# Kernel tuning notes

Measured on AMD Instinct MI355X. Metric: run time of the kernel, lower is better.

## Reference

```python
import jax, jax.numpy as jnp
import numpy as np

NEG_SLOPE = 0.2


def gat_conv(x, src, dst, W, att_src, att_dst, bias, heads, out_ch, concat, N):
    # Linear transform: [N, heads, out_ch]
    h = (x @ W).reshape(N, heads, out_ch)
    # Per-node attention logits [N, heads]
    a_s = jnp.einsum('nhc,hc->nh', h, att_src)
    a_d = jnp.einsum('nhc,hc->nh', h, att_dst)
    # Per-edge logits: edge j->i uses src j, dst i
    e = jax.nn.leaky_relu(a_s[src] + a_d[dst], NEG_SLOPE)  # [E, heads]
    # Segment softmax over destination neighborhoods
    m = jax.ops.segment_max(e, dst, num_segments=N)  # [N, heads]
    ex = jnp.exp(e - m[dst])
    denom = jax.ops.segment_sum(ex, dst, num_segments=N)
    alpha = ex / denom[dst]  # [E, heads]
    # Weighted message scatter-add
    out = jax.ops.segment_sum(h[src] * alpha[:, :, None], dst, num_segments=N)  # [N, heads, out_ch]
    out = out.reshape(N, heads * out_ch) if concat else out.mean(axis=1)
    return out + bias


def setup_inputs() -> dict:
    key = jax.random.key(0)
    ks = jax.random.split(key, 12)
    N, E, F_IN, HID, HEADS, NCLS = 100000, 1600000, 256, 16, 8, 32
    x = jax.random.normal(ks[0], (N, F_IN), dtype=jnp.float32)
    edge_index = jax.random.randint(ks[1], (2, E), 0, N, dtype=jnp.int32)
    edge_weight = jax.random.uniform(ks[2], (E,), dtype=jnp.float32)
    s1 = 1.0 / np.sqrt(F_IN)
    W1 = jax.random.normal(ks[3], (F_IN, HEADS * HID), dtype=jnp.float32) * s1
    att_src1 = jax.random.normal(ks[4], (HEADS, HID), dtype=jnp.float32) * 0.1
    att_dst1 = jax.random.normal(ks[5], (HEADS, HID), dtype=jnp.float32) * 0.1
    b1 = jnp.zeros((HEADS * HID,), dtype=jnp.float32)
    s2 = 1.0 / np.sqrt(HEADS * HID)
    W2 = jax.random.normal(ks[6], (HEADS * HID, NCLS), dtype=jnp.float32) * s2
    att_src2 = jax.random.normal(ks[7], (1, NCLS), dtype=jnp.float32) * 0.1
    att_dst2 = jax.random.normal(ks[8], (1, NCLS), dtype=jnp.float32) * 0.1
    b2 = jnp.zeros((NCLS,), dtype=jnp.float32)
    return {"x": x, "edge_index": edge_index, "edge_weight": edge_weight,
            "W1": W1, "att_src1": att_src1, "att_dst1": att_dst1, "b1": b1,
            "W2": W2, "att_src2": att_src2, "att_dst2": att_dst2, "b2": b2}


def reference(x, edge_index, edge_weight, W1, att_src1, att_dst1, b1, W2, att_src2, att_dst2, b2):
    N = x.shape[0]
    # PyG GATConv add_self_loops=True: append self-loops once (used by both layers)
    loop = jnp.arange(N, dtype=edge_index.dtype)
    src = jnp.concatenate([edge_index[0], loop])
    dst = jnp.concatenate([edge_index[1], loop])
    # eval mode: dropout is identity; edge_weight unused by GATConv
    h = gat_conv(x, src, dst, W1, att_src1, att_dst1, b1, heads=8, out_ch=16, concat=True, N=N)
    h = jax.nn.elu(h)
    out = gat_conv(h, src, dst, W2, att_src2, att_dst2, b2, heads=1, out_ch=32, concat=False, N=N)
    return jax.nn.log_softmax(out, axis=-1)
```

## Files before the change

kernel.cpp:

```cpp
#include <hip/hip_runtime.h>
#include <hip/hip_fp16.h>
#include <math.h>

#define NEG_SLOPE 0.2f
#define NBLK 256

typedef _Float16 half8 __attribute__((ext_vector_type(8)));
typedef _Float16 half4 __attribute__((ext_vector_type(4)));
typedef float f32x4 __attribute__((ext_vector_type(4)));

__device__ __forceinline__ float lrelu(float x){ return x > 0.f ? x : NEG_SLOPE*x; }

__global__ void k_prepw(const float* __restrict__ W, _Float16* __restrict__ Wt){
  int t = blockIdx.x*blockDim.x + threadIdx.x;
  int c = t >> 8, k = t & 255;
  Wt[t] = (_Float16)W[k*128 + c];
}

__global__ __launch_bounds__(256) void k_gemm1(const float* __restrict__ x,
                                               const _Float16* __restrict__ Wt,
                                               _Float16* __restrict__ h1h, int N){
  __shared__ _Float16 aL[2][128*40];
  __shared__ _Float16 bL[2][128*40];
  int tid = threadIdx.x;
  int w = tid >> 6, lane = tid & 63;
  int fq = lane >> 4, fr = lane & 15;
  int row0 = blockIdx.x * 128;
  f32x4 acc[2][8];
  #pragma unroll
  for (int m=0;m<2;m++)
    #pragma unroll
    for (int n=0;n<8;n++) acc[m][n] = (f32x4){0.f,0.f,0.f,0.f};

  int rA = tid>>3, kcA = (tid&7)*4;
  float4 va[4]; half8 vb[2];

  #pragma unroll
  for (int it=0; it<4; it++){
    int gr = row0 + it*32 + rA;
    va[it] = make_float4(0.f,0.f,0.f,0.f);
    if (gr < N) va[it] = *(const float4*)&x[(size_t)gr*256 + kcA];
  }
  #pragma unroll
  for (int it=0; it<2; it++){
    int chunk = it*256 + tid;
    vb[it] = *(const half8*)&Wt[(size_t)(chunk>>2)*256 + (chunk&3)*8];
  }
  #pragma unroll
  for (int it=0; it<4; it++){
    half4 hv; hv[0]=(_Float16)va[it].x; hv[1]=(_Float16)va[it].y;
    hv[2]=(_Float16)va[it].z; hv[3]=(_Float16)va[it].w;
    *(half4*)&aL[0][(it*32+rA)*40 + kcA] = hv;
  }
  #pragma unroll
  for (int it=0; it<2; it++){
    int chunk = it*256 + tid;
    *(half8*)&bL[0][(chunk>>2)*40 + (chunk&3)*8] = vb[it];
  }
  __syncthreads();

  int cur = 0;
  for (int ki=0; ki<8; ki++){
    int kk = ki*32;
    if (ki < 7){
      #pragma unroll
      for (int it=0; it<4; it++){
        int gr = row0 + it*32 + rA;
        va[it] = make_float4(0.f,0.f,0.f,0.f);
        if (gr < N) va[it] = *(const float4*)&x[(size_t)gr*256 + kk + 32 + kcA];
      }
      #pragma unroll
      for (int it=0; it<2; it++){
        int chunk = it*256 + tid;
        vb[it] = *(const half8*)&Wt[(size_t)(chunk>>2)*256 + kk + 32 + (chunk&3)*8];
      }
    }
    int kb = fq*8;
    half8 afrag[2], bfrag[8];
    #pragma unroll
    for (int m=0;m<2;m++) afrag[m] = *(half8*)&aL[cur][(w*32 + m*16 + fr)*40 + kb];
    #pragma unroll
    for (int n=0;n<8;n++) bfrag[n] = *(half8*)&bL[cur][(n*16 + fr)*40 + kb];
    #pragma unroll
    for (int m=0;m<2;m++)
      #pragma unroll
      for (int n=0;n<8;n++)
        acc[m][n] = __builtin_amdgcn_mfma_f32_16x16x32_f16(afrag[m], bfrag[n], acc[m][n], 0, 0, 0);
    if (ki < 7){
      #pragma unroll
      for (int it=0; it<4; it++){
        half4 hv; hv[0]=(_Float16)va[it].x; hv[1]=(_Float16)va[it].y;
        hv[2]=(_Float16)va[it].z; hv[3]=(_Float16)va[it].w;
        *(half4*)&aL[cur^1][(it*32+rA)*40 + kcA] = hv;
      }
      #pragma unroll
      for (int it=0; it<2; it++){
        int chunk = it*256 + tid;
        *(half8*)&bL[cur^1][(chunk>>2)*40 + (chunk&3)*8] = vb[it];
      }
      __syncthreads();
      cur ^= 1;
    }
  }
  #pragma unroll
  for (int m=0;m<2;m++){
    #pragma unroll
    for (int j=0;j<4;j++){
      int gr = row0 + w*32 + m*16 + fq*4 + j;
      if (gr < N){
        #pragma unroll
        for (int n=0;n<8;n++)
          h1h[(size_t)gr*128 + n*16 + fr] = (_Float16)acc[m][n][j];
      }
    }
  }
}

__global__ void k_att1(const __half* __restrict__ h1h, const float* __restrict__ as_w,
                       const float* __restrict__ ad_w,
                       float* __restrict__ a_s, float* __restrict__ a_d, int N){
  int t = blockIdx.x*blockDim.x + threadIdx.x;
  if (t >= N*8) return;
  int n = t >> 3, h = t & 7;
  const __half* hp = &h1h[(size_t)n*128 + h*16];
  const float* wsp = &as_w[h*16];
  const float* wdp = &ad_w[h*16];
  float s=0.f, d=0.f;
  #pragma unroll
  for (int j=0;j<8;j++){
    __half2 hv = *(const __half2*)&hp[j*2];
    float2 f = __half22float2(hv);
    s = fmaf(f.x, wsp[j*2],   s); d = fmaf(f.x, wdp[j*2],   d);
    s = fmaf(f.y, wsp[j*2+1], s); d = fmaf(f.y, wdp[j*2+1], d);
  }
  a_s[t] = s; a_d[t] = d;
}

__global__ __launch_bounds__(256) void k_bh(const int* __restrict__ dst, int* __restrict__ bh,
                                            int E, int EE, int NB){
  __shared__ int h[1024];
  int tid = threadIdx.x, blk = blockIdx.x;
  for (int i=tid;i<1024;i+=256) h[i]=0;
  __syncthreads();
  int chunk = (EE + NBLK - 1)/NBLK;
  int e0 = blk*chunk, e1 = min(e0+chunk, EE);
  for (int e=e0+tid; e<e1; e+=256){
    int d = (e<E)? dst[e] : (e-E);
    atomicAdd(&h[d>>7], 1);
  }
  __syncthreads();
  for (int i=tid;i<NB;i+=256) bh[i*NBLK + blk] = h[i];
}

__global__ __launch_bounds__(256) void k_scanA(int* __restrict__ bh, int* __restrict__ btot){
  __shared__ int t[256];
  int b = blockIdx.x, tid = threadIdx.x;
  int v = bh[b*NBLK + tid];
  t[tid] = v;
  __syncthreads();
  for (int off=1; off<256; off<<=1){
    int p = (tid>=off)? t[tid-off] : 0;
    __syncthreads();
    t[tid] += p;
    __syncthreads();
  }
  bh[b*NBLK + tid] = t[tid] - v;
  if (tid==255) btot[b] = t[255];
}

__global__ __launch_bounds__(256) void k_bscan(const int* __restrict__ btot, int* __restrict__ bbase,
                                               int* __restrict__ start_, int NB, int N, int EE){
  __shared__ int t[256];
  int tid = threadIdx.x;
  int i0 = tid*4;
  int a0 = (i0+0<NB)? btot[i0+0] : 0;
  int a1 = (i0+1<NB)? btot[i0+1] : 0;
  int a2 = (i0+2<NB)? btot[i0+2] : 0;
  int a3 = (i0+3<NB)? btot[i0+3] : 0;
  int s = a0+a1+a2+a3;
  t[tid] = s;
  __syncthreads();
  for (int off=1; off<256; off<<=1){
    int p = (tid>=off)? t[tid-off] : 0;
    __syncthreads();
    t[tid] += p;
    __syncthreads();
  }
  int excl = t[tid] - s;
  int e0=excl, e1=e0+a0, e2=e1+a1, e3=e2+a2;
  if (i0+0<NB) bbase[i0+0]=e0;
  if (i0+1<NB) bbase[i0+1]=e1;
  if (i0+2<NB) bbase[i0+2]=e2;
  if (i0+3<NB) bbase[i0+3]=e3;
  if (tid==0){ bbase[NB] = EE; start_[N] = EE; }
}

__global__ __launch_bounds__(256) void k_bfill(const int* __restrict__ src, const int* __restrict__ dst,
                       const int* __restrict__ bh, const int* __restrict__ bbase,
                       uint2* __restrict__ pairs, int E, int EE, int NB){
  __shared__ int cur[1024];
  int tid = threadIdx.x, blk = blockIdx.x;
  for (int i=tid;i<NB;i+=256) cur[i] = bbase[i] + bh[i*NBLK + blk];
  __syncthreads();
  int chunk = (EE + NBLK - 1)/NBLK;
  int e0 = blk*chunk, e1 = min(e0+chunk, EE);
  for (int e=e0+tid; e<e1; e+=256){
    int s,d;
    if (e<E){ s=src[e]; d=dst[e]; } else { s=e-E; d=s; }
    int p = atomicAdd(&cur[d>>7], 1);
    pairs[p] = make_uint2((unsigned)s,(unsigned)d);
  }
}

__global__ __launch_bounds__(256) void k_pb(const int* __restrict__ bbase, const uint2* __restrict__ pairs,
                    int* __restrict__ start_, int* __restrict__ csr_src, int N){
  __shared__ int hist[128];
  __shared__ int excl[128];
  int b = blockIdx.x;
  int tid = threadIdx.x;
  int base = bbase[b], cnt = bbase[b+1] - base;
  if (tid<128) hist[tid]=0;
  __syncthreads();
  for (int i=tid;i<cnt;i+=256){
    uint2 p = pairs[base+i];
    atomicAdd(&hist[p.y & 127], 1);
  }
  __syncthreads();
  if (tid < 128) excl[tid] = hist[tid];
  __syncthreads();
  for (int off=1; off<128; off<<=1){
    int p=0;
    if (tid<128 && tid>=off) p = excl[tid-off];
    __syncthreads();
    if (tid<128) excl[tid] += p;
    __syncthreads();
  }
  if (tid < 128){
    int e = excl[tid] - hist[tid];
    int node = (b<<7) + tid;
    if (node < N) start_[node] = base + e;
    hist[tid] = e;
  }
  __syncthreads();
  for (int i=tid;i<cnt;i+=256){
    uint2 p = pairs[base+i];
    int pos = atomicAdd(&hist[p.y & 127], 1);
    csr_src[base + pos] = (int)p.x;
  }
}

__global__ __launch_bounds__(256) void k_agg1(const int* __restrict__ start, const int* __restrict__ csr_src,
                      const float* __restrict__ a_s, const float* __restrict__ a_d,
                      const __half* __restrict__ h1h, float* __restrict__ acc1, int N){
  int wid = (blockIdx.x*blockDim.x + threadIdx.x) >> 6;
  int lane = threadIdx.x & 63;
  if (wid >= N) return;
  int d = wid;
  int half = lane >> 5;
  int l32  = lane & 31;
  int head = l32 >> 2;
  float ad = a_d[(size_t)d*8 + head];
  int beg = start[d], end = start[d+1];
  float ax=0.f, ay=0.f, az=0.f, aw=0.f, den=0.f;
  int j = beg + half;
  for (; j + 6 < end; j += 8){
    int s0 = csr_src[j];
    int s1 = csr_src[j+2];
    int s2 = csr_src[j+4];
    int s3 = csr_src[j+6];
    float e0 = __expf(lrelu(a_s[(size_t)s0*8 + head] + ad));
    float e1 = __expf(lrelu(a_s[(size_t)s1*8 + head] + ad));
    float e2 = __expf(lrelu(a_s[(size_t)s2*8 + head] + ad));
    float e3 = __expf(lrelu(a_s[(size_t)s3*8 + head] + ad));
    float2 r0 = *(const float2*)&h1h[(size_t)s0*128 + l32*4];
    float2 r1 = *(const float2*)&h1h[(size_t)s1*128 + l32*4];
    float2 r2 = *(const float2*)&h1h[(size_t)s2*128 + l32*4];
    float2 r3 = *(const float2*)&h1h[(size_t)s3*128 + l32*4];
    float2 f0a = __half22float2(*(__half2*)&r0.x), f0b = __half22float2(*(__half2*)&r0.y);
    float2 f1a = __half22float2(*(__half2*)&r1.x), f1b = __half22float2(*(__half2*)&r1.y);
    float2 f2a = __half22float2(*(__half2*)&r2.x), f2b = __half22float2(*(__half2*)&r2.y);
    float2 f3a = __half22float2(*(__half2*)&r3.x), f3b = __half22float2(*(__half2*)&r3.y);
    ax = fmaf(e0, f0a.x, ax); ay = fmaf(e0, f0a.y, ay); az = fmaf(e0, f0b.x, az); aw = fmaf(e0, f0b.y, aw);
    ax = fmaf(e1, f1a.x, ax); ay = fmaf(e1, f1a.y, ay); az = fmaf(e1, f1b.x, az); aw = fmaf(e1, f1b.y, aw);
    ax = fmaf(e2, f2a.x, ax); ay = fmaf(e2, f2a.y, ay); az = fmaf(e2, f2b.x, az); aw = fmaf(e2, f2b.y, aw);
    ax = fmaf(e3, f3a.x, ax); ay = fmaf(e3, f3a.y, ay); az = fmaf(e3, f3b.x, az); aw = fmaf(e3, f3b.y, aw);
    den += (e0 + e1) + (e2 + e3);
  }
  for (; j < end; j += 2){
    int s0 = csr_src[j];
    float e0 = __expf(lrelu(a_s[(size_t)s0*8 + head] + ad));
    float2 r0 = *(const float2*)&h1h[(size_t)s0*128 + l32*4];
    float2 f0a = __half22float2(*(__half2*)&r0.x), f0b = __half22float2(*(__half2*)&r0.y);
    ax = fmaf(e0, f0a.x, ax); ay = fmaf(e0, f0a.y, ay); az = fmaf(e0, f0b.x, az); aw = fmaf(e0, f0b.y, aw);
    den += e0;
  }
  ax += __shfl_xor(ax, 32);
  ay += __shfl_xor(ay, 32);
  az += __shfl_xor(az, 32);
  aw += __shfl_xor(aw, 32);
  den += __shfl_xor(den, 32);
  float inv = (den > 0.f) ? 1.f/den : 0.f;
  if (half == 0){
    float4 o = make_float4(ax*inv, ay*inv, az*inv, aw*inv);
    *(float4*)&acc1[(size_t)d*128 + l32*4] = o;
  }
}

__global__ __launch_bounds__(256) void k_layer2(const float* __restrict__ acc1, const float* __restrict__ b1,
                        const float* __restrict__ W2, const float* __restrict__ as2w,
                        const float* __restrict__ ad2w,
                        __half* __restrict__ h2ph, float* __restrict__ a_s2,
                        float* __restrict__ a_d2, int N){
  __shared__ float w2s[128][32];
  __shared__ float hs[8][128];
  int tid = threadIdx.x;
  #pragma unroll
  for (int it=0; it<16; it++){
    int idx = it*256 + tid;
    ((float*)w2s)[idx] = W2[idx];
  }
  int sub = tid>>5, ln = tid&31;
  int n = blockIdx.x*8 + sub;
  if (n < N){
    #pragma unroll
    for (int j=0;j<4;j++){
      int k = j*32 + ln;
      float v = acc1[(size_t)n*128+k] + b1[k];
      hs[sub][k] = v > 0.f ? v : (__expf(v) - 1.f);
    }
  }
  __syncthreads();
  if (n >= N) return;
  float o = 0.f;
  #pragma unroll
  for (int k=0;k<128;k++) o = fmaf(hs[sub][k], w2s[k][ln], o);
  h2ph[(size_t)n*32+ln] = __float2half_rn(o);
  float ps = o*as2w[ln], pd = o*ad2w[ln];
  #pragma unroll
  for (int m=16;m;m>>=1){ ps += __shfl_xor(ps,m); pd += __shfl_xor(pd,m); }
  if (ln==0){ a_s2[n]=ps; a_d2[n]=pd; }
}

__global__ __launch_bounds__(256) void k_agg2(const int* __restrict__ start, const int* __restrict__ csr_src,
                      const float* __restrict__ a_s2, const float* __restrict__ a_d2,
                      const __half* __restrict__ h2ph, const float* __restrict__ b2,
                      float* __restrict__ out, int N){
  int g = (blockIdx.x*blockDim.x + threadIdx.x) >> 5;
  int ln = threadIdx.x & 31;
  if (g >= N) return;
  int d = g;
  int grp = ln >> 4;
  int l16 = ln & 15;
  float ad = a_d2[d];
  int beg = start[d], end = start[d+1];
  float accx=0.f, accy=0.f, den=0.f;
  int j = beg + grp;
  for (; j + 6 < end; j += 8){
    int s0 = csr_src[j];
    int s1 = csr_src[j+2];
    int s2 = csr_src[j+4];
    int s3 = csr_src[j+6];
    float e0 = __expf(lrelu(a_s2[s0] + ad));
    float e1 = __expf(lrelu(a_s2[s1] + ad));
    float e2 = __expf(lrelu(a_s2[s2] + ad));
    float e3 = __expf(lrelu(a_s2[s3] + ad));
    float2 v0 = __half22float2(*(const __half2*)&h2ph[(size_t)s0*32 + l16*2]);
    float2 v1 = __half22float2(*(const __half2*)&h2ph[(size_t)s1*32 + l16*2]);
    float2 v2 = __half22float2(*(const __half2*)&h2ph[(size_t)s2*32 + l16*2]);
    float2 v3 = __half22float2(*(const __half2*)&h2ph[(size_t)s3*32 + l16*2]);
    accx = fmaf(e0, v0.x, accx); accy = fmaf(e0, v0.y, accy);
    accx = fmaf(e1, v1.x, accx); accy = fmaf(e1, v1.y, accy);
    accx = fmaf(e2, v2.x, accx); accy = fmaf(e2, v2.y, accy);
    accx = fmaf(e3, v3.x, accx); accy = fmaf(e3, v3.y, accy);
    den += (e0 + e1) + (e2 + e3);
  }
  for (; j < end; j += 2){
    int s0 = csr_src[j];
    float e0 = __expf(lrelu(a_s2[s0] + ad));
    float2 v0 = __half22float2(*(const __half2*)&h2ph[(size_t)s0*32 + l16*2]);
    accx = fmaf(e0, v0.x, accx); accy = fmaf(e0, v0.y, accy);
    den += e0;
  }
  accx += __shfl_xor(accx, 16);
  accy += __shfl_xor(accy, 16);
  den  += __shfl_xor(den, 16);
  float2 bb = *(const float2*)&b2[l16*2];
  float vx = accx/den + bb.x;
  float vy = accy/den + bb.y;
  float mx = fmaxf(vx, vy);
  #pragma unroll
  for (int m=8;m;m>>=1) mx = fmaxf(mx, __shfl_xor(mx, m));
  float sm = __expf(vx-mx) + __expf(vy-mx);
  #pragma unroll
  for (int m=8;m;m>>=1) sm += __shfl_xor(sm, m);
  float lg = mx + __logf(sm);
  if (grp == 0){
    float2 o = make_float2(vx - lg, vy - lg);
    *(float2*)&out[(size_t)d*32 + l16*2] = o;
  }
}

extern "C" void kernel_launch(void* const* d_in, const int* in_sizes, int n_in,
                              void* d_out, int out_size, void* d_ws, size_t ws_size,
                              hipStream_t stream){
  const float* x   = (const float*)d_in[0];
  const int*   ei  = (const int*)d_in[1];
  const float* W1  = (const float*)d_in[3];
  const float* as1 = (const float*)d_in[4];
  const float* ad1 = (const float*)d_in[5];
  const float* b1  = (const float*)d_in[6];
  const float* W2  = (const float*)d_in[7];
  const float* as2 = (const float*)d_in[8];
  const float* ad2 = (const float*)d_in[9];
  const float* b2  = (const float*)d_in[10];

  int N  = in_sizes[0] / 256;
  int E  = in_sizes[2];
  int EE = E + N;
  const int* src = ei;
  const int* dst = ei + E;

  int NB = (N + 127) >> 7;

  int* iw = (int*)d_ws;
  int* bh      = iw;                 iw += 1024*NBLK;
  int* btot    = iw;                 iw += 1024;
  int* bbase   = iw;                 iw += 1028;
  int* start_  = iw;                 iw += ((N+1+3)/4)*4;
  int* csr_src = iw;                 iw += ((EE+3)/4)*4;

  float* w = (float*)iw;
  float* a_s1   = w; w += (size_t)N*8;
  float* a_d1   = w; w += (size_t)N*8;
  float* acc1   = w; w += (size_t)N*128;
  float* a_s2   = w; w += (size_t)N;
  float* a_d2   = w; w += (size_t)N;
  _Float16* h1h  = (_Float16*)w; w += (size_t)N*64;
  _Float16* h2ph = (_Float16*)w; w += (size_t)N*16;
  _Float16* Wt   = (_Float16*)w; w += 32768/2;
  float* out    = (float*)d_out;

  uint2* pairs = (uint2*)acc1;

  hipLaunchKernelGGL(k_prepw, dim3(128), dim3(256), 0, stream, W1, Wt);
  hipLaunchKernelGGL(k_gemm1, dim3((N+127)/128), dim3(256), 0, stream, x, Wt, h1h, N);
  hipLaunchKernelGGL(k_att1, dim3((N*8+255)/256), dim3(256), 0, stream, (const __half*)h1h, as1, ad1, a_s1, a_d1, N);
  hipLaunchKernelGGL(k_bh,    dim3(NBLK), dim3(256), 0, stream, dst, bh, E, EE, NB);
  hipLaunchKernelGGL(k_scanA, dim3(NB),   dim3(256), 0, stream, bh, btot);
  hipLaunchKernelGGL(k_bscan, dim3(1),    dim3(256), 0, stream, btot, bbase, start_, NB, N, EE);
  hipLaunchKernelGGL(k_bfill, dim3(NBLK), dim3(256), 0, stream, src, dst, bh, bbase, pairs, E, EE, NB);
  hipLaunchKernelGGL(k_pb,    dim3(NB),   dim3(256), 0, stream, bbase, pairs, start_, csr_src, N);
  hipLaunchKernelGGL(k_agg1, dim3((N+3)/4), dim3(256), 0, stream, start_, csr_src, a_s1, a_d1, (const __half*)h1h, acc1, N);
  hipLaunchKernelGGL(k_layer2, dim3((N+7)/8), dim3(256), 0, stream, acc1, b1, W2, as2, ad2, (__half*)h2ph, a_s2, a_d2, N);
  hipLaunchKernelGGL(k_agg2, dim3((N+7)/8), dim3(256), 0, stream, start_, csr_src, a_s2, a_d2, (const __half*)h2ph, b2, out, N);
}
```

Baseline: 292.1 us.

## Store layer-1 features as FP8 for gather, fp16 aggregate, packed 32-bit edge pairs

New measurement: 259.8 us. -11.0%, faster.

```diff
diff --git a/kernel.cpp b/kernel.cpp
--- a/kernel.cpp
+++ b/kernel.cpp
@@ -8,6 +8,7 @@
 typedef _Float16 half8 __attribute__((ext_vector_type(8)));
 typedef _Float16 half4 __attribute__((ext_vector_type(4)));
 typedef float f32x4 __attribute__((ext_vector_type(4)));
+typedef float f32x2 __attribute__((ext_vector_type(2)));
 
 __device__ __forceinline__ float lrelu(float x){ return x > 0.f ? x : NEG_SLOPE*x; }
 
@@ -116,24 +117,32 @@
   }
 }
 
-__global__ void k_att1(const __half* __restrict__ h1h, const float* __restrict__ as_w,
-                       const float* __restrict__ ad_w,
-                       float* __restrict__ a_s, float* __restrict__ a_d, int N){
+__global__ void k_cvt8(const _Float16* __restrict__ h1h,
+                       const float* __restrict__ as_w, const float* __restrict__ ad_w,
+                       unsigned* __restrict__ h1p, float* __restrict__ a_s,
+                       float* __restrict__ a_d, int N){
   int t = blockIdx.x*blockDim.x + threadIdx.x;
-  if (t >= N*8) return;
-  int n = t >> 3, h = t & 7;
-  const __half* hp = &h1h[(size_t)n*128 + h*16];
-  const float* wsp = &as_w[h*16];
-  const float* wdp = &ad_w[h*16];
+  if (t >= N*16) return;
+  int row = t >> 4, c8 = t & 15;
+  half8 hv = *(const half8*)&h1h[(size_t)row*128 + c8*8];
+  float f[8];
+  #pragma unroll
+  for (int j=0;j<8;j++) f[j] = (float)hv[j];
+  int w0 = 0, w1 = 0;
+  w0 = __builtin_amdgcn_cvt_pk_fp8_f32(f[0], f[1], w0, false);
+  w0 = __builtin_amdgcn_cvt_pk_fp8_f32(f[2], f[3], w0, true);
+  w1 = __builtin_amdgcn_cvt_pk_fp8_f32(f[4], f[5], w1, false);
+  w1 = __builtin_amdgcn_cvt_pk_fp8_f32(f[6], f[7], w1, true);
+  *(uint2*)&h1p[(size_t)row*32 + c8*2] = make_uint2((unsigned)w0,(unsigned)w1);
+  int head = c8 >> 1;
+  const float* wsp = &as_w[head*16 + (c8&1)*8];
+  const float* wdp = &ad_w[head*16 + (c8&1)*8];
   float s=0.f, d=0.f;
   #pragma unroll
-  for (int j=0;j<8;j++){
-    __half2 hv = *(const __half2*)&hp[j*2];
-    float2 f = __half22float2(hv);
-    s = fmaf(f.x, wsp[j*2],   s); d = fmaf(f.x, wdp[j*2],   d);
-    s = fmaf(f.y, wsp[j*2+1], s); d = fmaf(f.y, wdp[j*2+1], d);
-  }
-  a_s[t] = s; a_d[t] = d;
+  for (int j=0;j<8;j++){ s = fmaf(f[j], wsp[j], s); d = fmaf(f[j], wdp[j], d); }
+  s += __shfl_xor(s, 1);
+  d += __shfl_xor(d, 1);
+  if ((c8&1)==0){ a_s[(size_t)row*8+head]=s; a_d[(size_t)row*8+head]=d; }
 }
 
 __global__ __launch_bounds__(256) void k_bh(const int* __restrict__ dst, int* __restrict__ bh,
@@ -197,7 +206,7 @@
 
 __global__ __launch_bounds__(256) void k_bfill(const int* __restrict__ src, const int* __restrict__ dst,
                        const int* __restrict__ bh, const int* __restrict__ bbase,
-                       uint2* __restrict__ pairs, int E, int EE, int NB){
+                       unsigned* __restrict__ pairs, int E, int EE, int NB){
   __shared__ int cur[1024];
   int tid = threadIdx.x, blk = blockIdx.x;
   for (int i=tid;i<NB;i+=256) cur[i] = bbase[i] + bh[i*NBLK + blk];
@@ -208,11 +217,11 @@
     int s,d;
     if (e<E){ s=src[e]; d=dst[e]; } else { s=e-E; d=s; }
     int p = atomicAdd(&cur[d>>7], 1);
-    pairs[p] = make_uint2((unsigned)s,(unsigned)d);
-  }
-}
-
-__global__ __launch_bounds__(256) void k_pb(const int* __restrict__ bbase, const uint2* __restrict__ pairs,
+    pairs[p] = ((unsigned)s << 7) | (unsigned)(d & 127);
+  }
+}
+
+__global__ __launch_bounds__(256) void k_pb(const int* __restrict__ bbase, const unsigned* __restrict__ pairs,
                     int* __restrict__ start_, int* __restrict__ csr_src, int N){
   __shared__ int hist[128];
   __shared__ int excl[128];
@@ -222,8 +231,8 @@
   if (tid<128) hist[tid]=0;
   __syncthreads();
   for (int i=tid;i<cnt;i+=256){
-    uint2 p = pairs[base+i];
-    atomicAdd(&hist[p.y & 127], 1);
+    unsigned p = pairs[base+i];
+    atomicAdd(&hist[p & 127], 1);
   }
   __syncthreads();
   if (tid < 128) excl[tid] = hist[tid];
@@ -243,15 +252,15 @@
   }
   __syncthreads();
   for (int i=tid;i<cnt;i+=256){
-    uint2 p = pairs[base+i];
-    int pos = atomicAdd(&hist[p.y & 127], 1);
-    csr_src[base + pos] = (int)p.x;
+    unsigned p = pairs[base+i];
+    int pos = atomicAdd(&hist[p & 127], 1);
+    csr_src[base + pos] = (int)(p >> 7);
   }
 }
 
 __global__ __launch_bounds__(256) void k_agg1(const int* __restrict__ start, const int* __restrict__ csr_src,
                       const float* __restrict__ a_s, const float* __restrict__ a_d,
-                      const __half* __restrict__ h1h, float* __restrict__ acc1, int N){
+                      const unsigned* __restrict__ h1p, _Float16* __restrict__ acc1h, int N){
   int wid = (blockIdx.x*blockDim.x + threadIdx.x) >> 6;
   int lane = threadIdx.x & 63;
   if (wid >= N) return;
@@ -272,26 +281,26 @@
     float e1 = __expf(lrelu(a_s[(size_t)s1*8 + head] + ad));
     float e2 = __expf(lrelu(a_s[(size_t)s2*8 + head] + ad));
     float e3 = __expf(lrelu(a_s[(size_t)s3*8 + head] + ad));
-    float2 r0 = *(const float2*)&h1h[(size_t)s0*128 + l32*4];
-    float2 r1 = *(const float2*)&h1h[(size_t)s1*128 + l32*4];
-    float2 r2 = *(const float2*)&h1h[(size_t)s2*128 + l32*4];
-    float2 r3 = *(const float2*)&h1h[(size_t)s3*128 + l32*4];
-    float2 f0a = __half22float2(*(__half2*)&r0.x), f0b = __half22float2(*(__half2*)&r0.y);
-    float2 f1a = __half22float2(*(__half2*)&r1.x), f1b = __half22float2(*(__half2*)&r1.y);
-    float2 f2a = __half22float2(*(__half2*)&r2.x), f2b = __half22float2(*(__half2*)&r2.y);
-    float2 f3a = __half22float2(*(__half2*)&r3.x), f3b = __half22float2(*(__half2*)&r3.y);
-    ax = fmaf(e0, f0a.x, ax); ay = fmaf(e0, f0a.y, ay); az = fmaf(e0, f0b.x, az); aw = fmaf(e0, f0b.y, aw);
-    ax = fmaf(e1, f1a.x, ax); ay = fmaf(e1, f1a.y, ay); az = fmaf(e1, f1b.x, az); aw = fmaf(e1, f1b.y, aw);
-    ax = fmaf(e2, f2a.x, ax); ay = fmaf(e2, f2a.y, ay); az = fmaf(e2, f2b.x, az); aw = fmaf(e2, f2b.y, aw);
-    ax = fmaf(e3, f3a.x, ax); ay = fmaf(e3, f3a.y, ay); az = fmaf(e3, f3b.x, az); aw = fmaf(e3, f3b.y, aw);
+    unsigned u0 = h1p[(size_t)s0*32 + l32];
+    unsigned u1 = h1p[(size_t)s1*32 + l32];
+    unsigned u2 = h1p[(size_t)s2*32 + l32];
+    unsigned u3 = h1p[(size_t)s3*32 + l32];
+    f32x2 l0 = __builtin_amdgcn_cvt_pk_f32_fp8((int)u0, false), h0 = __builtin_amdgcn_cvt_pk_f32_fp8((int)u0, true);
+    f32x2 l1 = __builtin_amdgcn_cvt_pk_f32_fp8((int)u1, false), h1 = __builtin_amdgcn_cvt_pk_f32_fp8((int)u1, true);
+    f32x2 l2 = __builtin_amdgcn_cvt_pk_f32_fp8((int)u2, false), h2 = __builtin_amdgcn_cvt_pk_f32_fp8((int)u2, true);
+    f32x2 l3 = __builtin_amdgcn_cvt_pk_f32_fp8((int)u3, false), h3 = __builtin_amdgcn_cvt_pk_f32_fp8((int)u3, true);
+    ax = fmaf(e0, l0.x, ax); ay = fmaf(e0, l0.y, ay); az = fmaf(e0, h0.x, az); aw = fmaf(e0, h0.y, aw);
+    ax = fmaf(e1, l1.x, ax); ay = fmaf(e1, l1.y, ay); az = fmaf(e1, h1.x, az); aw = fmaf(e1, h1.y, aw);
+    ax = fmaf(e2, l2.x, ax); ay = fmaf(e2, l2.y, ay); az = fmaf(e2, h2.x, az); aw = fmaf(e2, h2.y, aw);
+    ax = fmaf(e3, l3.x, ax); ay = fmaf(e3, l3.y, ay); az = fmaf(e3, h3.x, az); aw = fmaf(e3, h3.y, aw);
     den += (e0 + e1) + (e2 + e3);
   }
   for (; j < end; j += 2){
     int s0 = csr_src[j];
     float e0 = __expf(lrelu(a_s[(size_t)s0*8 + head] + ad));
-    float2 r0 = *(const float2*)&h1h[(size_t)s0*128 + l32*4];
-    float2 f0a = __half22float2(*(__half2*)&r0.x), f0b = __half22float2(*(__half2*)&r0.y);
-    ax = fmaf(e0, f0a.x, ax); ay = fmaf(e0, f0a.y, ay); az = fmaf(e0, f0b.x, az); aw = fmaf(e0, f0b.y, aw);
+    unsigned u0 = h1p[(size_t)s0*32 + l32];
+    f32x2 l0 = __builtin_amdgcn_cvt_pk_f32_fp8((int)u0, false), h0 = __builtin_amdgcn_cvt_pk_f32_fp8((int)u0, true);
+    ax = fmaf(e0, l0.x, ax); ay = fmaf(e0, l0.y, ay); az = fmaf(e0, h0.x, az); aw = fmaf(e0, h0.y, aw);
     den += e0;
   }
   ax += __shfl_xor(ax, 32);
@@ -301,12 +310,14 @@
   den += __shfl_xor(den, 32);
   float inv = (den > 0.f) ? 1.f/den : 0.f;
   if (half == 0){
-    float4 o = make_float4(ax*inv, ay*inv, az*inv, aw*inv);
-    *(float4*)&acc1[(size_t)d*128 + l32*4] = o;
-  }
-}
-
-__global__ __launch_bounds__(256) void k_layer2(const float* __restrict__ acc1, const float* __restrict__ b1,
+    half4 o;
+    o[0]=(_Float16)(ax*inv); o[1]=(_Float16)(ay*inv);
+    o[2]=(_Float16)(az*inv); o[3]=(_Float16)(aw*inv);
+    *(half4*)&acc1h[(size_t)d*128 + l32*4] = o;
+  }
+}
+
+__global__ __launch_bounds__(256) void k_layer2(const _Float16* __restrict__ acc1h, const float* __restrict__ b1,
                         const float* __restrict__ W2, const float* __restrict__ as2w,
                         const float* __restrict__ ad2w,
                         __half* __restrict__ h2ph, float* __restrict__ a_s2,
@@ -322,12 +333,16 @@
   int sub = tid>>5, ln = tid&31;
   int n = blockIdx.x*8 + sub;
   if (n < N){
-    #pragma unroll
-    for (int j=0;j<4;j++){
-      int k = j*32 + ln;
-      float v = acc1[(size_t)n*128+k] + b1[k];
-      hs[sub][k] = v > 0.f ? v : (__expf(v) - 1.f);
-    }
+    half4 hv = *(const half4*)&acc1h[(size_t)n*128 + ln*4];
+    float4 bb = *(const float4*)&b1[ln*4];
+    float v0 = (float)hv[0] + bb.x;
+    float v1 = (float)hv[1] + bb.y;
+    float v2 = (float)hv[2] + bb.z;
+    float v3 = (float)hv[3] + bb.w;
+    hs[sub][ln*4+0] = v0 > 0.f ? v0 : (__expf(v0) - 1.f);
+    hs[sub][ln*4+1] = v1 > 0.f ? v1 : (__expf(v1) - 1.f);
+    hs[sub][ln*4+2] = v2 > 0.f ? v2 : (__expf(v2) - 1.f);
+    hs[sub][ln*4+3] = v3 > 0.f ? v3 : (__expf(v3) - 1.f);
   }
   __syncthreads();
   if (n >= N) return;
@@ -432,25 +447,26 @@
   float* w = (float*)iw;
   float* a_s1   = w; w += (size_t)N*8;
   float* a_d1   = w; w += (size_t)N*8;
-  float* acc1   = w; w += (size_t)N*128;
   float* a_s2   = w; w += (size_t)N;
   float* a_d2   = w; w += (size_t)N;
+  _Float16* acc1h = (_Float16*)w; w += (size_t)N*64;
   _Float16* h1h  = (_Float16*)w; w += (size_t)N*64;
   _Float16* h2ph = (_Float16*)w; w += (size_t)N*16;
   _Float16* Wt   = (_Float16*)w; w += 32768/2;
+  unsigned* h1p  = (unsigned*)w; w += (size_t)N*16;
   float* out    = (float*)d_out;
 
-  uint2* pairs = (uint2*)acc1;
+  unsigned* pairs = (unsigned*)acc1h;
 
   hipLaunchKernelGGL(k_prepw, dim3(128), dim3(256), 0, stream, W1, Wt);
   hipLaunchKernelGGL(k_gemm1, dim3((N+127)/128), dim3(256), 0, stream, x, Wt, h1h, N);
-  hipLaunchKernelGGL(k_att1, dim3((N*8+255)/256), dim3(256), 0, stream, (const __half*)h1h, as1, ad1, a_s1, a_d1, N);
+  hipLaunchKernelGGL(k_cvt8, dim3((N*16+255)/256), dim3(256), 0, stream, h1h, as1, ad1, h1p, a_s1, a_d1, N);
   hipLaunchKernelGGL(k_bh,    dim3(NBLK), dim3(256), 0, stream, dst, bh, E, EE, NB);
   hipLaunchKernelGGL(k_scanA, dim3(NB),   dim3(256), 0, stream, bh, btot);
   hipLaunchKernelGGL(k_bscan, dim3(1),    dim3(256), 0, stream, btot, bbase, start_, NB, N, EE);
   hipLaunchKernelGGL(k_bfill, dim3(NBLK), dim3(256), 0, stream, src, dst, bh, bbase, pairs, E, EE, NB);
   hipLaunchKernelGGL(k_pb,    dim3(NB),   dim3(256), 0, stream, bbase, pairs, start_, csr_src, N);
-  hipLaunchKernelGGL(k_agg1, dim3((N+3)/4), dim3(256), 0, stream, start_, csr_src, a_s1, a_d1, (const __half*)h1h, acc1, N);
-  hipLaunchKernelGGL(k_layer2, dim3((N+7)/8), dim3(256), 0, stream, acc1, b1, W2, as2, ad2, (__half*)h2ph, a_s2, a_d2, N);
+  hipLaunchKernelGGL(k_agg1, dim3((N+3)/4), dim3(256), 0, stream, start_, csr_src, a_s1, a_d1, h1p, acc1h, N);
+  hipLaunchKernelGGL(k_layer2, dim3((N+7)/8), dim3(256), 0, stream, acc1h, b1, W2, as2, ad2, (__half*)h2ph, a_s2, a_d2, N);
   hipLaunchKernelGGL(k_agg2, dim3((N+7)/8), dim3(256), 0, stream, start_, csr_src, a_s2, a_d2, (const __half*)h2ph, b2, out, N);
 }
```
